# Performance work log

Hardware: AMD Instinct MI355X
Metric: run time of the kernel (lower is better)

The kernel has to match this reference:

```python
import jax, jax.numpy as jnp
import numpy as np

N_NODES = 50000
N_EDGES = 800000
D = 128
N_LAYERS = 4
N_GRAPHS = 512
N_CLASS = 10


def setup_inputs() -> dict:
    key = jax.random.key(0)
    ks = jax.random.split(key, 12)
    x = jax.random.normal(ks[0], (N_NODES, D), dtype=jnp.float32)
    edge_index = jax.random.randint(ks[1], (2, N_EDGES), 0, N_NODES, dtype=jnp.int64)
    batch = jnp.sort(jax.random.randint(ks[2], (N_NODES,), 0, N_GRAPHS, dtype=jnp.int64))
    s = 1.0 / np.sqrt(D)
    W_conv = jax.random.uniform(ks[3], (N_LAYERS, D, D), jnp.float32, -s, s)
    b_conv = jnp.zeros((N_LAYERS, D), jnp.float32)
    W1 = jax.random.uniform(ks[4], (D, D), jnp.float32, -s, s)
    b1 = jnp.zeros((D,), jnp.float32)
    W2 = jax.random.uniform(ks[5], (D, D // 2), jnp.float32, -s, s)
    b2 = jnp.zeros((D // 2,), jnp.float32)
    W3 = jax.random.uniform(ks[6], (D // 2, N_CLASS), jnp.float32, -1.0 / np.sqrt(D // 2), 1.0 / np.sqrt(D // 2))
    b3 = jnp.zeros((N_CLASS,), jnp.float32)
    return {"x": x, "edge_index": edge_index, "batch": batch,
            "W_conv": W_conv, "b_conv": b_conv,
            "W1": W1, "b1": b1, "W2": W2, "b2": b2, "W3": W3, "b3": b3}


def reference(x, edge_index, batch, W_conv, b_conv, W1, b1, W2, b2, W3, b3):
    row, col = edge_index[0], edge_index[1]  # messages: source=row -> target=col
    # GCN symmetric normalization with self-loops (PyG GCNConv default).
    deg = jax.ops.segment_sum(jnp.ones((row.shape[0],), x.dtype), col, num_segments=N_NODES) + 1.0
    dinv = jax.lax.rsqrt(deg)
    edge_norm = (dinv[row] * dinv[col])[:, None]      # [E,1]
    self_norm = (1.0 / deg)[:, None]                  # [N,1] = dinv_i * dinv_i

    def gcn_layer(h, W, b):
        h = h @ W                                      # [N,D]
        agg = jax.ops.segment_sum(h[row] * edge_norm, col, num_segments=N_NODES)
        agg = agg + h * self_norm                      # self-loop contribution
        return jax.nn.relu(agg + b)

    h = x
    for l in range(N_LAYERS):
        h = gcn_layer(h, W_conv[l], b_conv[l])

    # global_add_pool over graph ids
    g = jax.ops.segment_sum(h, batch, num_segments=N_GRAPHS)  # [G,D]

    # MLP head (dropout is identity in eval mode)
    g = jax.nn.relu(g @ W1 + b1)
    g = jax.nn.relu(g @ W2 + b2)
    return g @ W3 + b3
```

## Files before the change

### kernel.cpp

```cpp
#include <hip/hip_runtime.h>
#include <stdint.h>
#include <stddef.h>

#define NN 50000
#define NE 800000
#define DD 128
#define NL 4
#define NG 512
#define NC 10
#define NB 196
#define BCAP 5056

using short8 = __attribute__((ext_vector_type(8))) short;
using f32x4  = __attribute__((ext_vector_type(4))) float;

__device__ __forceinline__ float bf2f(unsigned short u) {
  union { unsigned int i; float f; } c; c.i = ((unsigned int)u) << 16; return c.f;
}
__device__ __forceinline__ unsigned short f2bf(float f) {
  union { unsigned int i; float f; } c; c.f = f;
  unsigned int i = c.i;
  return (unsigned short)((i + 0x7FFFu + ((i >> 16) & 1u)) >> 16);
}
__device__ __forceinline__ unsigned int pack2(float a, float b) {
  return (unsigned int)f2bf(a) | ((unsigned int)f2bf(b) << 16);
}
__device__ __forceinline__ void acc8(float* a, uint4 p) {
  a[0] += bf2f((unsigned short)(p.x & 0xffffu)); a[1] += bf2f((unsigned short)(p.x >> 16));
  a[2] += bf2f((unsigned short)(p.y & 0xffffu)); a[3] += bf2f((unsigned short)(p.y >> 16));
  a[4] += bf2f((unsigned short)(p.z & 0xffffu)); a[5] += bf2f((unsigned short)(p.z >> 16));
  a[6] += bf2f((unsigned short)(p.w & 0xffffu)); a[7] += bf2f((unsigned short)(p.w >> 16));
}

__global__ __launch_bounds__(1024) void p1a_k(const int* __restrict__ ecol,
                                              int* __restrict__ hist) {
  __shared__ int lh[NB];
  int tid = threadIdx.x;
  if (tid < NB) lh[tid] = 0;
  __syncthreads();
  int e0 = blockIdx.x * 4096 + tid;
#pragma unroll
  for (int j = 0; j < 4; ++j) {
    int e = e0 + j * 1024;
    if (e < NE) atomicAdd(&lh[ecol[e] >> 8], 1);
  }
  __syncthreads();
  if (tid < NB && lh[tid] > 0) atomicAdd(&hist[tid], lh[tid]);
}

__global__ __launch_bounds__(256) void scanb_k(const int* __restrict__ hist,
                                               int* __restrict__ ebase,
                                               int* __restrict__ cursor,
                                               int* __restrict__ csr_ptr) {
  __shared__ int sc[256];
  int t = threadIdx.x;
  int h = (t < NB) ? hist[t] : 0;
  sc[t] = h; __syncthreads();
  for (int off = 1; off < 256; off <<= 1) {
    int v = (t >= off) ? sc[t - off] : 0;
    __syncthreads();
    sc[t] += v;
    __syncthreads();
  }
  if (t < NB) { ebase[t] = sc[t] - h; cursor[t] = sc[t] - h; }
  if (t == NB - 1) ebase[NB] = sc[t];
  if (t == 0) csr_ptr[NN] = NE;
}

__global__ __launch_bounds__(1024) void p1b_k(const int* __restrict__ erow,
                                              const int* __restrict__ ecol,
                                              int* __restrict__ cursor,
                                              unsigned int* __restrict__ ebuf) {
  __shared__ int lcnt[NB], gb[NB];
  int tid = threadIdx.x;
  if (tid < NB) lcnt[tid] = 0;
  __syncthreads();
  int e0 = blockIdx.x * 4096 + tid;
  int bk[4], sl[4]; unsigned int pk[4];
#pragma unroll
  for (int j = 0; j < 4; ++j) {
    int e = e0 + j * 1024;
    bk[j] = -1;
    if (e < NE) {
      int d = ecol[e], s = erow[e];
      bk[j] = d >> 8;
      pk[j] = ((unsigned int)(d & 255) << 16) | (unsigned int)s;
      sl[j] = atomicAdd(&lcnt[bk[j]], 1);
    }
  }
  __syncthreads();
  if (tid < NB) {
    int c = lcnt[tid];
    gb[tid] = c ? atomicAdd(&cursor[tid], c) : 0;
  }
  __syncthreads();
#pragma unroll
  for (int j = 0; j < 4; ++j)
    if (bk[j] >= 0) ebuf[gb[bk[j]] + sl[j]] = pk[j];
}

__global__ __launch_bounds__(1024) void p2_k(const unsigned int* __restrict__ ebuf,
                                             const int* __restrict__ ebase,
                                             const float* __restrict__ x,
                                             int* __restrict__ csr_ptr,
                                             int* __restrict__ csr_src,
                                             float* __restrict__ dinv,
                                             unsigned short* __restrict__ xb) {
  __shared__ unsigned int pr[BCAP];
  __shared__ int srcb[BCAP];
  __shared__ int hist_s[256], scn[256], lcur[256];
  __shared__ float dinv_s[256];
  int b = blockIdx.x, tid = threadIdx.x;
  int beg = ebase[b];
  int cnt = ebase[b + 1] - beg;
  if (cnt > BCAP) cnt = BCAP;

  if (tid < 256) hist_s[tid] = 0;
  __syncthreads();
  for (int i = tid; i < cnt; i += 1024) {
    unsigned int p = ebuf[beg + i];
    pr[i] = p;
    atomicAdd(&hist_s[p >> 16], 1);
  }
  __syncthreads();
  if (tid < 256) scn[tid] = hist_s[tid];
  __syncthreads();
  for (int off = 1; off < 256; off <<= 1) {
    int v = (tid < 256 && tid >= off) ? scn[tid - off] : 0;
    __syncthreads();
    if (tid < 256) scn[tid] += v;
    __syncthreads();
  }
  if (tid < 256) {
    int ex = scn[tid] - hist_s[tid];
    lcur[tid] = ex;
    int V = b * 256 + tid;
    if (V < NN) {
      csr_ptr[V] = beg + ex;
      float dv = rsqrtf((float)(hist_s[tid] + 1));
      dinv[V] = dv;
      dinv_s[tid] = dv;
    }
  }
  __syncthreads();
  for (int i = tid; i < cnt; i += 1024) {
    unsigned int p = pr[i];
    int pos = atomicAdd(&lcur[p >> 16], 1);
    srcb[pos] = (int)(p & 0xFFFFu);
  }
  __syncthreads();
  for (int i = tid; i < cnt; i += 1024) csr_src[beg + i] = srcb[i];

  for (int i4 = tid; i4 < 256 * 32; i4 += 1024) {
    int vl = i4 >> 5;
    int V = b * 256 + vl;
    if (V < NN) {
      float d = dinv_s[vl];
      f32x4 vx = *((const f32x4*)(x + (size_t)V * DD) + (i4 & 31));
      uint2 o;
      o.x = pack2(vx[0] * d, vx[1] * d);
      o.y = pack2(vx[2] * d, vx[3] * d);
      *((uint2*)(xb + (size_t)V * DD) + (i4 & 31)) = o;
    }
  }
}

__global__ void gptr_k(const int* __restrict__ batch, int* __restrict__ gptr) {
  int i = blockIdx.x * 256 + threadIdx.x;
  if (i >= NN) return;
  int b  = batch[i];
  int bp = (i == 0) ? -1 : batch[i - 1];
  for (int g = bp + 1; g <= b; ++g) gptr[g] = i;
  if (i == NN - 1) { for (int g = b + 1; g <= NG; ++g) gptr[g] = NN; }
}

__global__ __launch_bounds__(256) void agg_k(const unsigned short* __restrict__ hs,
                                             unsigned short* __restrict__ agg,
                                             const int* __restrict__ csr_ptr,
                                             const int* __restrict__ csr_src,
                                             const float* __restrict__ dinv) {
  int v = blockIdx.x * 4 + (threadIdx.x >> 6);
  if (v >= NN) return;
  int lane = threadIdx.x & 63;
  int qg = lane >> 4, r = lane & 15;
  const uint4* rows = (const uint4*)hs;

  float a[8] = {0.f, 0.f, 0.f, 0.f, 0.f, 0.f, 0.f, 0.f};
  float b[8] = {0.f, 0.f, 0.f, 0.f, 0.f, 0.f, 0.f, 0.f};
  if (qg == 0) acc8(a, rows[(size_t)v * 16 + r]);

  int e = csr_ptr[v] + qg, end = csr_ptr[v + 1];
  for (; e + 12 < end; e += 16) {
    int s0 = csr_src[e];
    int s1 = csr_src[e + 4];
    int s2 = csr_src[e + 8];
    int s3 = csr_src[e + 12];
    uint4 p0 = rows[(size_t)s0 * 16 + r];
    uint4 p1 = rows[(size_t)s1 * 16 + r];
    uint4 p2 = rows[(size_t)s2 * 16 + r];
    uint4 p3 = rows[(size_t)s3 * 16 + r];
    acc8(a, p0); acc8(b, p1); acc8(a, p2); acc8(b, p3);
  }
  for (; e + 4 < end; e += 8) {
    int s0 = csr_src[e];
    int s1 = csr_src[e + 4];
    uint4 p0 = rows[(size_t)s0 * 16 + r];
    uint4 p1 = rows[(size_t)s1 * 16 + r];
    acc8(a, p0); acc8(b, p1);
  }
  if (e < end) acc8(a, rows[(size_t)csr_src[e] * 16 + r]);

#pragma unroll
  for (int t = 0; t < 8; ++t) a[t] += b[t];

#pragma unroll
  for (int t = 0; t < 8; ++t) {
    a[t] += __shfl_xor(a[t], 16, 64);
    a[t] += __shfl_xor(a[t], 32, 64);
  }

  if (qg == 0) {
    float dv = dinv[v];
    uint4 o;
    o.x = pack2(dv * a[0], dv * a[1]);
    o.y = pack2(dv * a[2], dv * a[3]);
    o.z = pack2(dv * a[4], dv * a[5]);
    o.w = pack2(dv * a[6], dv * a[7]);
    *((uint4*)(agg + (size_t)v * DD) + r) = o;
  }
}

__global__ __launch_bounds__(256) void gemm_relu_k(const unsigned short* __restrict__ A,
                                                   const float* __restrict__ W,
                                                   const float* __restrict__ bias,
                                                   unsigned short* __restrict__ out,
                                                   const float* __restrict__ dscale,
                                                   int M) {
  __shared__ unsigned short Wt[128][136];
  int tid = threadIdx.x;
  for (int i = tid; i < 128 * 128; i += 256) {
    int k = i >> 7, n = i & 127;
    Wt[n][k] = f2bf(W[i]);
  }
  __syncthreads();

  int wave = tid >> 6, lane = tid & 63;
  int q = lane >> 4, r = lane & 15;
  int row0 = blockIdx.x * 64 + wave * 16;

  int arow = row0 + r;
  if (arow > M - 1) arow = M - 1;
  const short* Arow = (const short*)A + (size_t)arow * DD;

  short8 afrag[4];
#pragma unroll
  for (int ks = 0; ks < 4; ++ks)
    afrag[ks] = *(const short8*)(Arow + ks * 32 + q * 8);

  f32x4 acc[8];
#pragma unroll
  for (int ct = 0; ct < 8; ++ct) acc[ct] = (f32x4){0.f, 0.f, 0.f, 0.f};

#pragma unroll
  for (int ks = 0; ks < 4; ++ks) {
#pragma unroll
    for (int ct = 0; ct < 8; ++ct) {
      short8 bfrag = *(const short8*)(&Wt[ct * 16 + r][ks * 32 + q * 8]);
      acc[ct] = __builtin_amdgcn_mfma_f32_16x16x32_bf16(afrag[ks], bfrag, acc[ct], 0, 0, 0);
    }
  }

  int orow = row0 + q * 4;
  float sc[4];
#pragma unroll
  for (int reg = 0; reg < 4; ++reg) {
    int rr = orow + reg;
    sc[reg] = (dscale && rr < M) ? dscale[rr] : 1.f;
  }
#pragma unroll
  for (int ct = 0; ct < 8; ++ct) {
    int coln = ct * 16 + r;
    float bc = bias[coln];
#pragma unroll
    for (int reg = 0; reg < 4; ++reg) {
      int rr = orow + reg;
      if (rr < M) {
        float val = fmaxf(acc[ct][reg] + bc, 0.f) * sc[reg];
        out[(size_t)rr * DD + coln] = f2bf(val);
      }
    }
  }
}

__global__ __launch_bounds__(128) void pool_k(const unsigned short* __restrict__ h,
                                              const int* __restrict__ gptr,
                                              float* __restrict__ gpool) {
  int g = blockIdx.x, t = threadIdx.x;
  int beg = gptr[g], end = gptr[g + 1];
  float acc = 0.f;
  for (int v = beg; v < end; ++v) acc += bf2f(h[(size_t)v * DD + t]);
  gpool[g * DD + t] = acc;
}

__global__ __launch_bounds__(128) void mlp_k(const float* __restrict__ gpool,
                                             const float* __restrict__ W1,
                                             const float* __restrict__ b1,
                                             const float* __restrict__ W2,
                                             const float* __restrict__ b2,
                                             const float* __restrict__ W3,
                                             const float* __restrict__ b3,
                                             float* __restrict__ out) {
  __shared__ float s_g[128], s_h1[128], s_h2[64];
  int g = blockIdx.x, t = threadIdx.x;
  s_g[t] = gpool[g * DD + t];
  __syncthreads();
  {
    float a = b1[t];
    for (int k = 0; k < 128; ++k) a += s_g[k] * W1[k * 128 + t];
    s_h1[t] = fmaxf(a, 0.f);
  }
  __syncthreads();
  if (t < 64) {
    float a = b2[t];
    for (int k = 0; k < 128; ++k) a += s_h1[k] * W2[k * 64 + t];
    s_h2[t] = fmaxf(a, 0.f);
  }
  __syncthreads();
  if (t < NC) {
    float a = b3[t];
    for (int k = 0; k < 64; ++k) a += s_h2[k] * W3[k * NC + t];
    out[g * NC + t] = a;
  }
}


extern "C" void kernel_launch(void* const* d_in, const int* in_sizes, int n_in,
                              void* d_out, int out_size, void* d_ws, size_t ws_size,
                              hipStream_t stream) {
  const float* x     = (const float*)d_in[0];
  const int*   ei    = (const int*)d_in[1];
  const int*   batch = (const int*)d_in[2];
  const float* Wc    = (const float*)d_in[3];
  const float* bc    = (const float*)d_in[4];
  const float* W1    = (const float*)d_in[5];
  const float* b1    = (const float*)d_in[6];
  const float* W2    = (const float*)d_in[7];
  const float* b2    = (const float*)d_in[8];
  const float* W3    = (const float*)d_in[9];
  const float* b3    = (const float*)d_in[10];
  float* out = (float*)d_out;

  const int* erow = ei;
  const int* ecol = ei + NE;

  char* w = (char*)d_ws;
  int*   hist    = (int*)w;    w += NB * 4;
  int*   cursor  = (int*)w;    w += NB * 4;
  int*   ebase   = (int*)w;    w += (NB + 4) * 4;
  int*   csr_ptr = (int*)w;    w += (size_t)(NN + 4) * 4;
  int*   gptr    = (int*)w;    w += (NG + 4) * 4;
  int*   csr_src = (int*)w;    w += (size_t)NE * 4;
  float* dinv    = (float*)w;  w += (size_t)NN * 4;
  float* gpool   = (float*)w;  w += (size_t)NG * DD * 4;
  w = (char*)(((uintptr_t)w + 255) & ~(uintptr_t)255);
  unsigned short* xb   = (unsigned short*)w; w += (size_t)NN * DD * 2;
  unsigned short* aggb = (unsigned short*)w; w += (size_t)NN * DD * 2;
  unsigned short* hbuf = (unsigned short*)w; w += (size_t)NN * DD * 2;
  unsigned int* ebuf = (unsigned int*)aggb;

  hipMemsetAsync(d_ws, 0, NB * 2 * 4, stream);

  p1a_k  <<<NB, 1024, 0, stream>>>(ecol, hist);
  scanb_k<<<1, 256, 0, stream>>>(hist, ebase, cursor, csr_ptr);
  p1b_k  <<<NB, 1024, 0, stream>>>(erow, ecol, cursor, ebuf);
  p2_k   <<<NB, 1024, 0, stream>>>(ebuf, ebase, x, csr_ptr, csr_src, dinv, xb);
  gptr_k <<<(NN + 255) / 256, 256, 0, stream>>>(batch, gptr);

  const int aggGrid  = (NN + 3) / 4;
  const int gemmGrid = (NN + 63) / 64;

  for (int l = 0; l < NL; ++l) {
    const unsigned short* hin = (l == 0) ? xb : hbuf;
    const float* dsc = (l == NL - 1) ? nullptr : dinv;
    agg_k<<<aggGrid, 256, 0, stream>>>(hin, aggb, csr_ptr, csr_src, dinv);
    gemm_relu_k<<<gemmGrid, 256, 0, stream>>>(aggb, Wc + (size_t)l * DD * DD,
                                              bc + (size_t)l * DD, hbuf, dsc, NN);
  }

  pool_k<<<NG, 128, 0, stream>>>(hbuf, gptr, gpool);
  mlp_k <<<NG, 128, 0, stream>>>(gpool, W1, b1, W2, b2, W3, b3, out);

  (void)in_sizes; (void)n_in; (void)out_size; (void)ws_size;
}
```

Baseline: 365.6 us.

## Store node features in column-sliced layout so aggregation gathers stay cache-local

Node features are now stored as four column slices of 32 bf16 values each, written by the prep kernel and by the GEMM epilogue. The aggregation kernel gives each block a single slice, and each node is handled by four lanes reading 16 bytes per neighbor, with no cross-lane reduction. The aim is to shrink the working set of each random gather to a quarter of the feature matrix for better L2/MALL hit rates, and to remove the shuffle reduction. In exchange, the GEMM epilogue writes strided scattered 2-byte stores, gather accesses per edge are narrower (64 bytes per node per slice), and the per-node loop has less memory-level parallelism.

```diff
diff --git a/kernel.cpp b/kernel.cpp
--- a/kernel.cpp
+++ b/kernel.cpp
@@ -105,7 +105,7 @@
                                              int* __restrict__ csr_ptr,
                                              int* __restrict__ csr_src,
                                              float* __restrict__ dinv,
-                                             unsigned short* __restrict__ xb) {
+                                             unsigned short* __restrict__ xbT) {
   __shared__ unsigned int pr[BCAP];
   __shared__ int srcb[BCAP];
   __shared__ int hist_s[256], scn[256], lcur[256];
@@ -156,11 +156,13 @@
     int V = b * 256 + vl;
     if (V < NN) {
       float d = dinv_s[vl];
-      f32x4 vx = *((const f32x4*)(x + (size_t)V * DD) + (i4 & 31));
+      int q = i4 & 31;
+      f32x4 vx = *((const f32x4*)(x + (size_t)V * DD) + q);
       uint2 o;
       o.x = pack2(vx[0] * d, vx[1] * d);
       o.y = pack2(vx[2] * d, vx[3] * d);
-      *((uint2*)(xb + (size_t)V * DD) + (i4 & 31)) = o;
+      int sl = q >> 3;
+      ((uint2*)xbT)[((size_t)sl * NN + V) * 8 + (q & 7)] = o;
     }
   }
 }
@@ -174,60 +176,40 @@
   if (i == NN - 1) { for (int g = b + 1; g <= NG; ++g) gptr[g] = NN; }
 }
 
-__global__ __launch_bounds__(256) void agg_k(const unsigned short* __restrict__ hs,
+__global__ __launch_bounds__(256) void agg_k(const unsigned short* __restrict__ hsT,
                                              unsigned short* __restrict__ agg,
                                              const int* __restrict__ csr_ptr,
                                              const int* __restrict__ csr_src,
                                              const float* __restrict__ dinv) {
-  int v = blockIdx.x * 4 + (threadIdx.x >> 6);
-  if (v >= NN) return;
+  int s = blockIdx.x & 3;
+  int chunk = blockIdx.x >> 2;
   int lane = threadIdx.x & 63;
-  int qg = lane >> 4, r = lane & 15;
-  const uint4* rows = (const uint4*)hs;
-
-  float a[8] = {0.f, 0.f, 0.f, 0.f, 0.f, 0.f, 0.f, 0.f};
-  float b[8] = {0.f, 0.f, 0.f, 0.f, 0.f, 0.f, 0.f, 0.f};
-  if (qg == 0) acc8(a, rows[(size_t)v * 16 + r]);
-
-  int e = csr_ptr[v] + qg, end = csr_ptr[v + 1];
-  for (; e + 12 < end; e += 16) {
-    int s0 = csr_src[e];
-    int s1 = csr_src[e + 4];
-    int s2 = csr_src[e + 8];
-    int s3 = csr_src[e + 12];
-    uint4 p0 = rows[(size_t)s0 * 16 + r];
-    uint4 p1 = rows[(size_t)s1 * 16 + r];
-    uint4 p2 = rows[(size_t)s2 * 16 + r];
-    uint4 p3 = rows[(size_t)s3 * 16 + r];
-    acc8(a, p0); acc8(b, p1); acc8(a, p2); acc8(b, p3);
-  }
-  for (; e + 4 < end; e += 8) {
-    int s0 = csr_src[e];
-    int s1 = csr_src[e + 4];
-    uint4 p0 = rows[(size_t)s0 * 16 + r];
-    uint4 p1 = rows[(size_t)s1 * 16 + r];
+  int wave = threadIdx.x >> 6;
+  int n = chunk * 64 + wave * 16 + (lane >> 2);
+  int p = lane & 3;
+  if (n >= NN) return;
+  const uint4* base = (const uint4*)hsT + (size_t)s * NN * 4;
+
+  float a[8] = {0.f,0.f,0.f,0.f,0.f,0.f,0.f,0.f};
+  float b[8] = {0.f,0.f,0.f,0.f,0.f,0.f,0.f,0.f};
+  acc8(a, base[(size_t)n * 4 + p]);
+  int e = csr_ptr[n], end = csr_ptr[n + 1];
+  for (; e + 1 < end; e += 2) {
+    int s0 = csr_src[e], s1 = csr_src[e + 1];
+    uint4 p0 = base[(size_t)s0 * 4 + p];
+    uint4 p1 = base[(size_t)s1 * 4 + p];
     acc8(a, p0); acc8(b, p1);
   }
-  if (e < end) acc8(a, rows[(size_t)csr_src[e] * 16 + r]);
-
-#pragma unroll
-  for (int t = 0; t < 8; ++t) a[t] += b[t];
-
-#pragma unroll
-  for (int t = 0; t < 8; ++t) {
-    a[t] += __shfl_xor(a[t], 16, 64);
-    a[t] += __shfl_xor(a[t], 32, 64);
-  }
-
-  if (qg == 0) {
-    float dv = dinv[v];
-    uint4 o;
-    o.x = pack2(dv * a[0], dv * a[1]);
-    o.y = pack2(dv * a[2], dv * a[3]);
-    o.z = pack2(dv * a[4], dv * a[5]);
-    o.w = pack2(dv * a[6], dv * a[7]);
-    *((uint4*)(agg + (size_t)v * DD) + r) = o;
-  }
+  if (e < end) acc8(a, base[(size_t)csr_src[e] * 4 + p]);
+
+  float dv = dinv[n];
+#pragma unroll
+  for (int t = 0; t < 8; ++t) a[t] = (a[t] + b[t]) * dv;
+
+  uint4 o;
+  o.x = pack2(a[0], a[1]); o.y = pack2(a[2], a[3]);
+  o.z = pack2(a[4], a[5]); o.w = pack2(a[6], a[7]);
+  ((uint4*)(agg + (size_t)n * DD))[s * 4 + p] = o;
 }
 
 __global__ __launch_bounds__(256) void gemm_relu_k(const unsigned short* __restrict__ A,
@@ -235,7 +217,7 @@
                                                    const float* __restrict__ bias,
                                                    unsigned short* __restrict__ out,
                                                    const float* __restrict__ dscale,
-                                                   int M) {
+                                                   int M, int sliced) {
   __shared__ unsigned short Wt[128][136];
   int tid = threadIdx.x;
   for (int i = tid; i < 128 * 128; i += 256) {
@@ -281,12 +263,15 @@
   for (int ct = 0; ct < 8; ++ct) {
     int coln = ct * 16 + r;
     float bc = bias[coln];
+    size_t sbase = ((size_t)(ct >> 1) * NN) * 32 + (size_t)((ct & 1) * 16 + r);
 #pragma unroll
     for (int reg = 0; reg < 4; ++reg) {
       int rr = orow + reg;
       if (rr < M) {
         float val = fmaxf(acc[ct][reg] + bc, 0.f) * sc[reg];
-        out[(size_t)rr * DD + coln] = f2bf(val);
+        unsigned short bv = f2bf(val);
+        if (sliced) out[sbase + (size_t)rr * 32] = bv;
+        else        out[(size_t)rr * DD + coln] = bv;
       }
     }
   }
@@ -363,31 +348,34 @@
   float* dinv    = (float*)w;  w += (size_t)NN * 4;
   float* gpool   = (float*)w;  w += (size_t)NG * DD * 4;
   w = (char*)(((uintptr_t)w + 255) & ~(uintptr_t)255);
-  unsigned short* xb   = (unsigned short*)w; w += (size_t)NN * DD * 2;
+  unsigned short* xbT  = (unsigned short*)w; w += (size_t)NN * DD * 2;
   unsigned short* aggb = (unsigned short*)w; w += (size_t)NN * DD * 2;
-  unsigned short* hbuf = (unsigned short*)w; w += (size_t)NN * DD * 2;
-  unsigned int* ebuf = (unsigned int*)aggb;
+  unsigned short* hT   = (unsigned short*)w; w += (size_t)NN * DD * 2;
+  unsigned short* hRM  = (unsigned short*)w; w += (size_t)NN * DD * 2;
+  unsigned int* ebuf = (unsigned int*)hT;
 
   hipMemsetAsync(d_ws, 0, NB * 2 * 4, stream);
 
   p1a_k  <<<NB, 1024, 0, stream>>>(ecol, hist);
   scanb_k<<<1, 256, 0, stream>>>(hist, ebase, cursor, csr_ptr);
   p1b_k  <<<NB, 1024, 0, stream>>>(erow, ecol, cursor, ebuf);
-  p2_k   <<<NB, 1024, 0, stream>>>(ebuf, ebase, x, csr_ptr, csr_src, dinv, xb);
+  p2_k   <<<NB, 1024, 0, stream>>>(ebuf, ebase, x, csr_ptr, csr_src, dinv, xbT);
   gptr_k <<<(NN + 255) / 256, 256, 0, stream>>>(batch, gptr);
 
-  const int aggGrid  = (NN + 3) / 4;
+  const int aggGrid  = ((NN + 63) / 64) * 4;
   const int gemmGrid = (NN + 63) / 64;
 
   for (int l = 0; l < NL; ++l) {
-    const unsigned short* hin = (l == 0) ? xb : hbuf;
-    const float* dsc = (l == NL - 1) ? nullptr : dinv;
+    const unsigned short* hin = (l == 0) ? xbT : hT;
+    int last = (l == NL - 1);
     agg_k<<<aggGrid, 256, 0, stream>>>(hin, aggb, csr_ptr, csr_src, dinv);
     gemm_relu_k<<<gemmGrid, 256, 0, stream>>>(aggb, Wc + (size_t)l * DD * DD,
-                                              bc + (size_t)l * DD, hbuf, dsc, NN);
-  }
-
-  pool_k<<<NG, 128, 0, stream>>>(hbuf, gptr, gpool);
+                                              bc + (size_t)l * DD,
+                                              last ? hRM : hT,
+                                              last ? nullptr : dinv, NN, last ? 0 : 1);
+  }
+
+  pool_k<<<NG, 128, 0, stream>>>(hRM, gptr, gpool);
   mlp_k <<<NG, 128, 0, stream>>>(gpool, W1, b1, W2, b2, W3, b3, out);
 
   (void)in_sizes; (void)n_in; (void)out_size; (void)ws_size;
```

Result: no change. 366.1 us (+0.1%).

## Fold setup kernels, pre-transpose bf16 weights once, fuse pool with MLP

Applied to the files above, without the earlier changes.

Replaces the global-atomic histogram and its memset with per-block histogram rows that the scan kernel sums. The graph-pointer build and a one-time bf16 transpose of all conv weights become extra blocks of the CSR-build kernel. The GEMM then loads pre-transposed bf16 weights with vector loads instead of converting and transposing per block. Pooling and the MLP head are merged into one kernel. Together this removes several launches, a memset and redundant per-block weight conversion, at the cost of a serial 196-step sum in the single-block scan.

```diff
diff --git a/kernel.cpp b/kernel.cpp
--- a/kernel.cpp
+++ b/kernel.cpp
@@ -10,6 +10,7 @@
 #define NC 10
 #define NB 196
 #define BCAP 5056
+#define GPB 49
 
 using short8 = __attribute__((ext_vector_type(8))) short;
 using f32x4  = __attribute__((ext_vector_type(4))) float;
@@ -33,7 +34,7 @@
 }
 
 __global__ __launch_bounds__(1024) void p1a_k(const int* __restrict__ ecol,
-                                              int* __restrict__ hist) {
+                                              int* __restrict__ histM) {
   __shared__ int lh[NB];
   int tid = threadIdx.x;
   if (tid < NB) lh[tid] = 0;
@@ -45,16 +46,17 @@
     if (e < NE) atomicAdd(&lh[ecol[e] >> 8], 1);
   }
   __syncthreads();
-  if (tid < NB && lh[tid] > 0) atomicAdd(&hist[tid], lh[tid]);
-}
-
-__global__ __launch_bounds__(256) void scanb_k(const int* __restrict__ hist,
+  if (tid < 256) histM[blockIdx.x * 256 + tid] = (tid < NB) ? lh[tid] : 0;
+}
+
+__global__ __launch_bounds__(256) void scanb_k(const int* __restrict__ histM,
                                                int* __restrict__ ebase,
                                                int* __restrict__ cursor,
                                                int* __restrict__ csr_ptr) {
   __shared__ int sc[256];
   int t = threadIdx.x;
-  int h = (t < NB) ? hist[t] : 0;
+  int h = 0;
+  for (int b = 0; b < NB; ++b) h += histM[b * 256 + t];
   sc[t] = h; __syncthreads();
   for (int off = 1; off < 256; off <<= 1) {
     int v = (t >= off) ? sc[t - off] : 0;
@@ -102,15 +104,39 @@
 __global__ __launch_bounds__(1024) void p2_k(const unsigned int* __restrict__ ebuf,
                                              const int* __restrict__ ebase,
                                              const float* __restrict__ x,
+                                             const int* __restrict__ batch,
+                                             const float* __restrict__ Wc,
                                              int* __restrict__ csr_ptr,
                                              int* __restrict__ csr_src,
                                              float* __restrict__ dinv,
-                                             unsigned short* __restrict__ xb) {
+                                             unsigned short* __restrict__ xb,
+                                             int* __restrict__ gptr,
+                                             unsigned short* __restrict__ Wbt) {
+  int b = blockIdx.x, tid = threadIdx.x;
+  if (b >= NB + GPB) {
+    int l = b - NB - GPB;
+    const float* W = Wc + (size_t)l * DD * DD;
+    unsigned short* WT = Wbt + (size_t)l * DD * DD;
+    for (int i = tid; i < DD * DD; i += 1024) {
+      int n = i >> 7, k = i & 127;
+      WT[n * DD + k] = f2bf(W[k * DD + n]);
+    }
+    return;
+  }
+  if (b >= NB) {
+    int i = (b - NB) * 1024 + tid;
+    if (i >= NN) return;
+    int bb = batch[i];
+    int bp = (i == 0) ? -1 : batch[i - 1];
+    for (int g = bp + 1; g <= bb; ++g) gptr[g] = i;
+    if (i == NN - 1) { for (int g = bb + 1; g <= NG; ++g) gptr[g] = NN; }
+    return;
+  }
+
   __shared__ unsigned int pr[BCAP];
   __shared__ int srcb[BCAP];
   __shared__ int hist_s[256], scn[256], lcur[256];
   __shared__ float dinv_s[256];
-  int b = blockIdx.x, tid = threadIdx.x;
   int beg = ebase[b];
   int cnt = ebase[b + 1] - beg;
   if (cnt > BCAP) cnt = BCAP;
@@ -156,22 +182,14 @@
     int V = b * 256 + vl;
     if (V < NN) {
       float d = dinv_s[vl];
-      f32x4 vx = *((const f32x4*)(x + (size_t)V * DD) + (i4 & 31));
+      int q = i4 & 31;
+      f32x4 vx = *((const f32x4*)(x + (size_t)V * DD) + q);
       uint2 o;
       o.x = pack2(vx[0] * d, vx[1] * d);
       o.y = pack2(vx[2] * d, vx[3] * d);
-      *((uint2*)(xb + (size_t)V * DD) + (i4 & 31)) = o;
-    }
-  }
-}
-
-__global__ void gptr_k(const int* __restrict__ batch, int* __restrict__ gptr) {
-  int i = blockIdx.x * 256 + threadIdx.x;
-  if (i >= NN) return;
-  int b  = batch[i];
-  int bp = (i == 0) ? -1 : batch[i - 1];
-  for (int g = bp + 1; g <= b; ++g) gptr[g] = i;
-  if (i == NN - 1) { for (int g = b + 1; g <= NG; ++g) gptr[g] = NN; }
+      ((uint2*)(xb + (size_t)V * DD))[q] = o;
+    }
+  }
 }
 
 __global__ __launch_bounds__(256) void agg_k(const unsigned short* __restrict__ hs,
@@ -231,16 +249,16 @@
 }
 
 __global__ __launch_bounds__(256) void gemm_relu_k(const unsigned short* __restrict__ A,
-                                                   const float* __restrict__ W,
+                                                   const unsigned short* __restrict__ Wb,
                                                    const float* __restrict__ bias,
                                                    unsigned short* __restrict__ out,
                                                    const float* __restrict__ dscale,
                                                    int M) {
   __shared__ unsigned short Wt[128][136];
   int tid = threadIdx.x;
-  for (int i = tid; i < 128 * 128; i += 256) {
-    int k = i >> 7, n = i & 127;
-    Wt[n][k] = f2bf(W[i]);
+  for (int i = tid; i < 128 * 16; i += 256) {
+    int rr = i >> 4, c = i & 15;
+    *(uint4*)&Wt[rr][c * 8] = *(const uint4*)(Wb + rr * DD + c * 8);
   }
   __syncthreads();
 
@@ -292,27 +310,21 @@
   }
 }
 
-__global__ __launch_bounds__(128) void pool_k(const unsigned short* __restrict__ h,
-                                              const int* __restrict__ gptr,
-                                              float* __restrict__ gpool) {
+__global__ __launch_bounds__(128) void poolmlp_k(const unsigned short* __restrict__ h,
+                                                 const int* __restrict__ gptr,
+                                                 const float* __restrict__ W1,
+                                                 const float* __restrict__ b1,
+                                                 const float* __restrict__ W2,
+                                                 const float* __restrict__ b2,
+                                                 const float* __restrict__ W3,
+                                                 const float* __restrict__ b3,
+                                                 float* __restrict__ out) {
+  __shared__ float s_g[128], s_h1[128], s_h2[64];
   int g = blockIdx.x, t = threadIdx.x;
   int beg = gptr[g], end = gptr[g + 1];
   float acc = 0.f;
   for (int v = beg; v < end; ++v) acc += bf2f(h[(size_t)v * DD + t]);
-  gpool[g * DD + t] = acc;
-}
-
-__global__ __launch_bounds__(128) void mlp_k(const float* __restrict__ gpool,
-                                             const float* __restrict__ W1,
-                                             const float* __restrict__ b1,
-                                             const float* __restrict__ W2,
-                                             const float* __restrict__ b2,
-                                             const float* __restrict__ W3,
-                                             const float* __restrict__ b3,
-                                             float* __restrict__ out) {
-  __shared__ float s_g[128], s_h1[128], s_h2[64];
-  int g = blockIdx.x, t = threadIdx.x;
-  s_g[t] = gpool[g * DD + t];
+  s_g[t] = acc;
   __syncthreads();
   {
     float a = b1[t];
@@ -354,27 +366,25 @@
   const int* ecol = ei + NE;
 
   char* w = (char*)d_ws;
-  int*   hist    = (int*)w;    w += NB * 4;
+  int*   histM   = (int*)w;    w += (size_t)NB * 256 * 4;
   int*   cursor  = (int*)w;    w += NB * 4;
   int*   ebase   = (int*)w;    w += (NB + 4) * 4;
   int*   csr_ptr = (int*)w;    w += (size_t)(NN + 4) * 4;
   int*   gptr    = (int*)w;    w += (NG + 4) * 4;
   int*   csr_src = (int*)w;    w += (size_t)NE * 4;
   float* dinv    = (float*)w;  w += (size_t)NN * 4;
-  float* gpool   = (float*)w;  w += (size_t)NG * DD * 4;
   w = (char*)(((uintptr_t)w + 255) & ~(uintptr_t)255);
+  unsigned short* Wbt  = (unsigned short*)w; w += (size_t)NL * DD * DD * 2;
   unsigned short* xb   = (unsigned short*)w; w += (size_t)NN * DD * 2;
   unsigned short* aggb = (unsigned short*)w; w += (size_t)NN * DD * 2;
   unsigned short* hbuf = (unsigned short*)w; w += (size_t)NN * DD * 2;
   unsigned int* ebuf = (unsigned int*)aggb;
 
-  hipMemsetAsync(d_ws, 0, NB * 2 * 4, stream);
-
-  p1a_k  <<<NB, 1024, 0, stream>>>(ecol, hist);
-  scanb_k<<<1, 256, 0, stream>>>(hist, ebase, cursor, csr_ptr);
+  p1a_k  <<<NB, 1024, 0, stream>>>(ecol, histM);
+  scanb_k<<<1, 256, 0, stream>>>(histM, ebase, cursor, csr_ptr);
   p1b_k  <<<NB, 1024, 0, stream>>>(erow, ecol, cursor, ebuf);
-  p2_k   <<<NB, 1024, 0, stream>>>(ebuf, ebase, x, csr_ptr, csr_src, dinv, xb);
-  gptr_k <<<(NN + 255) / 256, 256, 0, stream>>>(batch, gptr);
+  p2_k   <<<NB + GPB + NL, 1024, 0, stream>>>(ebuf, ebase, x, batch, Wc, csr_ptr,
+                                              csr_src, dinv, xb, gptr, Wbt);
 
   const int aggGrid  = (NN + 3) / 4;
   const int gemmGrid = (NN + 63) / 64;
@@ -383,12 +393,11 @@
     const unsigned short* hin = (l == 0) ? xb : hbuf;
     const float* dsc = (l == NL - 1) ? nullptr : dinv;
     agg_k<<<aggGrid, 256, 0, stream>>>(hin, aggb, csr_ptr, csr_src, dinv);
-    gemm_relu_k<<<gemmGrid, 256, 0, stream>>>(aggb, Wc + (size_t)l * DD * DD,
+    gemm_relu_k<<<gemmGrid, 256, 0, stream>>>(aggb, Wbt + (size_t)l * DD * DD,
                                               bc + (size_t)l * DD, hbuf, dsc, NN);
   }
 
-  pool_k<<<NG, 128, 0, stream>>>(hbuf, gptr, gpool);
-  mlp_k <<<NG, 128, 0, stream>>>(gpool, W1, b1, W2, b2, W3, b3, out);
+  poolmlp_k<<<NG, 128, 0, stream>>>(hbuf, gptr, W1, b1, W2, b2, W3, b3, out);
 
   (void)in_sizes; (void)n_in; (void)out_size; (void)ws_size;
 }
```

Result: faster. 347.8 us (-4.9%).
